# Kernel optimization log

Hardware: AMD Instinct MI355X
Metric: run time of the kernel (lower is better)

The kernel has to match this reference:

```python
import jax, jax.numpy as jnp
import numpy as np

KNOTS = 17

def _buffers():
    t = jnp.linspace(0.0, 3.0, KNOTS)                # (K,)
    dt = 3.0 / (KNOTS - 1)
    w = jnp.full((KNOTS,), 2.0 * dt)
    w = w.at[jnp.array([0, KNOTS - 1])].set(dt)      # trapezoid-like weights
    phi = jnp.exp(-t * t / 2.0)                      # standard normal CF
    return t, phi, w * phi


def setup_inputs() -> dict:
    key = jax.random.key(0)
    kz, ka = jax.random.split(key)
    n, d, num_proj = 8192, 768, 1024
    z = jax.random.normal(kz, (n, d), dtype=jnp.float32)
    a = jax.random.normal(ka, (d, num_proj), dtype=jnp.float32)
    return {"z": z, "a": a}


def reference(z, a):
    t, phi, weights = _buffers()
    # normalize projection directions (columns of a) to unit L2 norm
    a_n = a / jnp.linalg.norm(a, axis=0, keepdims=True)          # (d, P)
    proj = z @ a_n                                               # (n, P)
    x_t = proj[..., None] * t                                    # (n, P, K)
    cos_mean = jnp.cos(x_t).mean(axis=-3)                        # (P, K)
    sin_mean = jnp.sin(x_t).mean(axis=-3)                        # (P, K)
    err = (cos_mean - phi) ** 2 + sin_mean ** 2                  # (P, K)
    n = z.shape[-2]
    return (err @ weights * n).mean()                            # scalar
```

## Files before the change

kernel.cpp:

```cpp
#include <hip/hip_runtime.h>
#include <math.h>

typedef __attribute__((ext_vector_type(8))) short bf16x8;
typedef __attribute__((ext_vector_type(4))) float f32x4;

#define N_ROWS 8192
#define D_DIM  768
#define P_DIM  1024
#define KNOTS  17
#define NK     16
#define NCH    128
#define KSTEPS 12
#define ALD    72

__device__ inline unsigned short f2bf(float f) {
    union { float f; unsigned int u; } x; x.f = f;
    unsigned int r = x.u + 0x7FFFu + ((x.u >> 16) & 1u);
    return (unsigned short)(r >> 16);
}

__device__ inline bf16x8 pack8(float4 a, float4 b) {
    union { unsigned short s[8]; bf16x8 v; } r;
    r.s[0] = f2bf(a.x); r.s[1] = f2bf(a.y); r.s[2] = f2bf(a.z); r.s[3] = f2bf(a.w);
    r.s[4] = f2bf(b.x); r.s[5] = f2bf(b.y); r.s[6] = f2bf(b.z); r.s[7] = f2bf(b.w);
    return r.v;
}

__device__ inline void gload_lds16(const unsigned short* g, const unsigned short* l) {
    auto gp = reinterpret_cast<const __attribute__((address_space(1))) char*>(
        reinterpret_cast<uintptr_t>(g));
    auto lp = reinterpret_cast<__attribute__((address_space(3))) char*>(
        (uintptr_t)(unsigned int)reinterpret_cast<uintptr_t>(l));
    __builtin_amdgcn_global_load_lds(gp, lp, 16, 0, 0);
}

__global__ __launch_bounds__(256) void colsq_kernel(const float* __restrict__ a,
                                                    float* __restrict__ cpart) {
    int p  = blockIdx.x * 256 + threadIdx.x;
    int d0 = blockIdx.y * 64;
    float s = 0.f;
    for (int d = 0; d < 64; ++d) {
        float v = a[(size_t)(d0 + d) * P_DIM + p];
        s = fmaf(v, v, s);
    }
    cpart[(size_t)blockIdx.y * P_DIM + p] = s;
}

__global__ __launch_bounds__(256) void atconv_kernel(const float* __restrict__ a,
                                                     const float* __restrict__ cpart,
                                                     unsigned short* __restrict__ Bt) {
    __shared__ float tile[64][65];
    __shared__ float linv[64];
    const int d0 = blockIdx.x * 64, p0 = blockIdx.y * 64;
    const int tid = threadIdx.x;
    if (tid < 64) {
        float s = 0.f;
        #pragma unroll
        for (int j = 0; j < D_DIM / 64; ++j)
            s += cpart[(size_t)j * P_DIM + p0 + tid];
        linv[tid] = rsqrtf(s);
    }
    #pragma unroll
    for (int pass = 0; pass < 16; ++pass) {
        int idx = pass * 256 + tid;
        int dr = idx >> 6, pc = idx & 63;
        tile[dr][pc] = a[(size_t)(d0 + dr) * P_DIM + p0 + pc];
    }
    __syncthreads();
    #pragma unroll
    for (int pass = 0; pass < 16; ++pass) {
        int idx = pass * 256 + tid;
        int pr = idx >> 6, dc = idx & 63;
        Bt[(size_t)(p0 + pr) * D_DIM + d0 + dc] = f2bf(tile[dc][pr] * linv[pr]);
    }
}

__global__ __launch_bounds__(512, 4) void gemmcf_kernel(const float* __restrict__ Z,
                                                        const unsigned short* __restrict__ B,
                                                        float* __restrict__ part) {
    __shared__ unsigned short AsB[2][128 * ALD];
    __shared__ unsigned short BsB[2][128 * 64];
    const int tid  = threadIdx.x;
    const int lane = tid & 63;
    const int wave = tid >> 6;
    const int wr = wave >> 2, wc = wave & 3;

    const int bid = blockIdx.x + blockIdx.y * 8;
    const int swz = (bid & 7) * 64 + (bid >> 3);
    const int bx = swz & 7, by = swz >> 3;
    const int row0 = by * 128;
    const int col0 = bx * 128;

    const int aR = wave * 16 + (lane >> 2);
    const int ac = lane & 3;
    const float* Zg = Z + (size_t)(row0 + aR) * D_DIM + ac * 8;

    const int srow = wave * 16 + (lane >> 3);
    const int sc   = (lane & 7) ^ ((lane >> 3) & 7);
    const unsigned short* Bg = B + (size_t)(col0 + srow) * D_DIM + sc * 8;
    const int ldsw = wave * 16 * 64;

    float4 ar0, ar1, ar2, ar3;

#define ALOAD(kt) do { const float* zp_ = Zg + (kt) * 64;                    \
        ar0 = *reinterpret_cast<const float4*>(zp_);                         \
        ar1 = *reinterpret_cast<const float4*>(zp_ + 4);                     \
        ar2 = *reinterpret_cast<const float4*>(zp_ + 32);                    \
        ar3 = *reinterpret_cast<const float4*>(zp_ + 36); } while (0)
#define AWRITE(db) do {                                                      \
        *reinterpret_cast<bf16x8*>(&AsB[db][aR * ALD + ac * 8])       = pack8(ar0, ar1); \
        *reinterpret_cast<bf16x8*>(&AsB[db][aR * ALD + (ac + 4) * 8]) = pack8(ar2, ar3); } while (0)
#define BSTAGE(kt, db) do { const int k0_ = (kt) * 64;                       \
        gload_lds16(Bg + k0_,             &BsB[db][ldsw]);                   \
        gload_lds16(Bg + k0_ + 8 * D_DIM, &BsB[db][ldsw + 8 * 64]); } while (0)
#define DRAIN_BARRIER() do {                                                 \
        asm volatile("s_waitcnt vmcnt(0) lgkmcnt(0)" ::: "memory");          \
        __builtin_amdgcn_sched_barrier(0);                                   \
        __builtin_amdgcn_s_barrier(); } while (0)

    f32x4 acc[4][2] = {};

    ALOAD(0);
    AWRITE(0);
    BSTAGE(0, 0);
    ALOAD(1);
    DRAIN_BARRIER();

    #pragma unroll
    for (int t = 0; t < KSTEPS; ++t) {
        const int cur = t & 1;
        if (t + 1 < KSTEPS) {
            AWRITE(cur ^ 1);
            BSTAGE(t + 1, cur ^ 1);
            if (t + 2 < KSTEPS) ALOAD(t + 2);
        }
        #pragma unroll
        for (int kk = 0; kk < 2; ++kk) {
            bf16x8 af[4], bfr[2];
            const int kg = kk * 4 + (lane >> 4);
            const int kbp = (kg ^ (lane & 7)) * 8;
            #pragma unroll
            for (int mi = 0; mi < 4; ++mi)
                af[mi] = *reinterpret_cast<const bf16x8*>(
                    &AsB[cur][(wr * 64 + mi * 16 + (lane & 15)) * ALD + kg * 8]);
            #pragma unroll
            for (int ni = 0; ni < 2; ++ni)
                bfr[ni] = *reinterpret_cast<const bf16x8*>(
                    &BsB[cur][(wc * 32 + ni * 16 + (lane & 15)) * 64 + kbp]);
            #pragma unroll
            for (int mi = 0; mi < 4; ++mi)
                #pragma unroll
                for (int ni = 0; ni < 2; ++ni)
                    acc[mi][ni] = __builtin_amdgcn_mfma_f32_16x16x32_bf16(
                        af[mi], bfr[ni], acc[mi][ni], 0, 0, 0);
        }
        if (t + 1 < KSTEPS) DRAIN_BARRIER();
    }
#undef ALOAD
#undef AWRITE
#undef BSTAGE
#undef DRAIN_BARRIER

    const float dt = 0.1875f;
    #pragma unroll
    for (int ni = 0; ni < 2; ++ni) {
        float cs[NK], ss[NK];
        #pragma unroll
        for (int k = 0; k < NK; ++k) { cs[k] = 0.f; ss[k] = 0.f; }
        #pragma unroll
        for (int mi = 0; mi < 4; ++mi)
            #pragma unroll
            for (int j = 0; j < 4; ++j) {
                float th = acc[mi][ni][j] * dt;
                float s1 = __sinf(th);
                float c1 = __cosf(th);
                float c2 = 2.f * c1;
                float ckm2 = 1.f, skm2 = 0.f;
                float ckm1 = c1,  skm1 = s1;
                cs[0] += c1; ss[0] += s1;
                #pragma unroll
                for (int k = 2; k <= NK; ++k) {
                    float ck = fmaf(c2, ckm1, -ckm2);
                    float sk = fmaf(c2, skm1, -skm2);
                    cs[k - 1] += ck; ss[k - 1] += sk;
                    ckm2 = ckm1; skm2 = skm1;
                    ckm1 = ck;   skm1 = sk;
                }
            }
        #pragma unroll
        for (int k = 0; k < NK; ++k) {
            cs[k] += __shfl_xor(cs[k], 16);
            cs[k] += __shfl_xor(cs[k], 32);
            ss[k] += __shfl_xor(ss[k], 16);
            ss[k] += __shfl_xor(ss[k], 32);
        }
        if (lane < 16) {
            int col = col0 + wc * 32 + ni * 16 + lane;
            size_t base = ((size_t)(by * 2 + wr) * 2 * NK) * P_DIM + col;
            #pragma unroll
            for (int k = 0; k < NK; ++k) {
                part[base + (size_t)k * P_DIM]        = cs[k];
                part[base + (size_t)(NK + k) * P_DIM] = ss[k];
            }
        }
    }
}

__global__ __launch_bounds__(256) void red1_kernel(const float* __restrict__ part,
                                                   float* __restrict__ sums) {
    int g = blockIdx.x * 256 + threadIdx.x;
    float s = 0.f;
    for (int c = 0; c < NCH; ++c)
        s += part[(size_t)c * 2 * NK * P_DIM + g];
    sums[g] = s;
}

__global__ __launch_bounds__(1024) void red2_kernel(const float* __restrict__ sums,
                                                    float* __restrict__ out) {
    const int p = threadIdx.x;
    const float dt = 0.1875f;
    const float inv_n = 1.0f / (float)N_ROWS;
    float contrib = 0.f;
    #pragma unroll
    for (int k = 1; k <= NK; ++k) {
        float cm   = sums[(k - 1) * P_DIM + p] * inv_n;
        float sm   = sums[(NK + k - 1) * P_DIM + p] * inv_n;
        float tk   = dt * (float)k;
        float phik = expf(-0.5f * tk * tk);
        float wk   = (k == KNOTS - 1) ? dt : 2.f * dt;
        float d    = cm - phik;
        contrib += wk * phik * (d * d + sm * sm);
    }
    __shared__ float red[1024];
    red[p] = contrib;
    __syncthreads();
    for (int sft = 512; sft > 0; sft >>= 1) {
        if (p < sft) red[p] += red[p + sft];
        __syncthreads();
    }
    if (p == 0) out[0] = red[0] * (float)N_ROWS / (float)P_DIM;
}

extern "C" void kernel_launch(void* const* d_in, const int* in_sizes, int n_in,
                              void* d_out, int out_size, void* d_ws, size_t ws_size,
                              hipStream_t stream) {
    const float* z = (const float*)d_in[0];
    const float* a = (const float*)d_in[1];
    float* out = (float*)d_out;

    char* ws = (char*)d_ws;
    float*          cpart = (float*)ws;
    unsigned short* Bt    = (unsigned short*)(ws + 65536);
    float*          part  = (float*)(ws + 65536 + 1572864);
    float*          sums  = (float*)(ws + 65536 + 1572864 + 16777216);

    colsq_kernel<<<dim3(P_DIM / 256, D_DIM / 64), 256, 0, stream>>>(a, cpart);
    atconv_kernel<<<dim3(D_DIM / 64, P_DIM / 64), 256, 0, stream>>>(a, cpart, Bt);
    gemmcf_kernel<<<dim3(P_DIM / 128, N_ROWS / 128), 512, 0, stream>>>(z, Bt, part);
    red1_kernel<<<dim3(2 * NK * P_DIM / 256), 256, 0, stream>>>(part, sums);
    red2_kernel<<<1, 1024, 0, stream>>>(sums, out);
}
```

Measured before the change: 119.5 us.

## Load B fragments directly from global into registers, dropping LDS staging

Removes the LDS double buffer for the B operand. Each wave now loads its bf16 B fragments straight from global memory into registers every k-step. The barrier waits only on LDS counters, and the next A prefetch moves after the MFMAs. The fp32 to bf16 packing also switches to the HIP intrinsic. This cuts LDS traffic and the vmcnt drain at each barrier. In exchange, B global-load latency is exposed inside the loop with no prefetch, and waves sharing columns load the same data redundantly.

```diff
diff --git a/kernel.cpp b/kernel.cpp
--- a/kernel.cpp
+++ b/kernel.cpp
@@ -1,4 +1,5 @@
 #include <hip/hip_runtime.h>
+#include <hip/hip_bf16.h>
 #include <math.h>
 
 typedef __attribute__((ext_vector_type(8))) short bf16x8;
@@ -19,19 +20,16 @@
     return (unsigned short)(r >> 16);
 }
 
+__device__ inline unsigned short bfbits(float f) {
+    union { __hip_bfloat16 h; unsigned short u; } c;
+    c.h = __float2bfloat16(f);
+    return c.u;
+}
 __device__ inline bf16x8 pack8(float4 a, float4 b) {
     union { unsigned short s[8]; bf16x8 v; } r;
-    r.s[0] = f2bf(a.x); r.s[1] = f2bf(a.y); r.s[2] = f2bf(a.z); r.s[3] = f2bf(a.w);
-    r.s[4] = f2bf(b.x); r.s[5] = f2bf(b.y); r.s[6] = f2bf(b.z); r.s[7] = f2bf(b.w);
+    r.s[0] = bfbits(a.x); r.s[1] = bfbits(a.y); r.s[2] = bfbits(a.z); r.s[3] = bfbits(a.w);
+    r.s[4] = bfbits(b.x); r.s[5] = bfbits(b.y); r.s[6] = bfbits(b.z); r.s[7] = bfbits(b.w);
     return r.v;
-}
-
-__device__ inline void gload_lds16(const unsigned short* g, const unsigned short* l) {
-    auto gp = reinterpret_cast<const __attribute__((address_space(1))) char*>(
-        reinterpret_cast<uintptr_t>(g));
-    auto lp = reinterpret_cast<__attribute__((address_space(3))) char*>(
-        (uintptr_t)(unsigned int)reinterpret_cast<uintptr_t>(l));
-    __builtin_amdgcn_global_load_lds(gp, lp, 16, 0, 0);
 }
 
 __global__ __launch_bounds__(256) void colsq_kernel(const float* __restrict__ a,
@@ -79,7 +77,6 @@
                                                         const unsigned short* __restrict__ B,
                                                         float* __restrict__ part) {
     __shared__ unsigned short AsB[2][128 * ALD];
-    __shared__ unsigned short BsB[2][128 * 64];
     const int tid  = threadIdx.x;
     const int lane = tid & 63;
     const int wave = tid >> 6;
@@ -95,10 +92,9 @@
     const int ac = lane & 3;
     const float* Zg = Z + (size_t)(row0 + aR) * D_DIM + ac * 8;
 
-    const int srow = wave * 16 + (lane >> 3);
-    const int sc   = (lane & 7) ^ ((lane >> 3) & 7);
-    const unsigned short* Bg = B + (size_t)(col0 + srow) * D_DIM + sc * 8;
-    const int ldsw = wave * 16 * 64;
+    const unsigned short* Bg0 =
+        B + (size_t)(col0 + wc * 32 + (lane & 15)) * D_DIM + (lane >> 4) * 8;
+    const unsigned short* Bg1 = Bg0 + (size_t)16 * D_DIM;
 
     float4 ar0, ar1, ar2, ar3;
 
@@ -110,11 +106,8 @@
 #define AWRITE(db) do {                                                      \
         *reinterpret_cast<bf16x8*>(&AsB[db][aR * ALD + ac * 8])       = pack8(ar0, ar1); \
         *reinterpret_cast<bf16x8*>(&AsB[db][aR * ALD + (ac + 4) * 8]) = pack8(ar2, ar3); } while (0)
-#define BSTAGE(kt, db) do { const int k0_ = (kt) * 64;                       \
-        gload_lds16(Bg + k0_,             &BsB[db][ldsw]);                   \
-        gload_lds16(Bg + k0_ + 8 * D_DIM, &BsB[db][ldsw + 8 * 64]); } while (0)
-#define DRAIN_BARRIER() do {                                                 \
-        asm volatile("s_waitcnt vmcnt(0) lgkmcnt(0)" ::: "memory");          \
+#define LGKM_BARRIER() do {                                                  \
+        asm volatile("s_waitcnt lgkmcnt(0)" ::: "memory");                   \
         __builtin_amdgcn_sched_barrier(0);                                   \
         __builtin_amdgcn_s_barrier(); } while (0)
 
@@ -122,44 +115,41 @@
 
     ALOAD(0);
     AWRITE(0);
-    BSTAGE(0, 0);
     ALOAD(1);
-    DRAIN_BARRIER();
+    LGKM_BARRIER();
 
     #pragma unroll
     for (int t = 0; t < KSTEPS; ++t) {
         const int cur = t & 1;
-        if (t + 1 < KSTEPS) {
-            AWRITE(cur ^ 1);
-            BSTAGE(t + 1, cur ^ 1);
-            if (t + 2 < KSTEPS) ALOAD(t + 2);
-        }
+        if (t + 1 < KSTEPS) AWRITE(cur ^ 1);
+        const bf16x8 b00 = *reinterpret_cast<const bf16x8*>(Bg0 + t * 64);
+        const bf16x8 b01 = *reinterpret_cast<const bf16x8*>(Bg1 + t * 64);
+        const bf16x8 b10 = *reinterpret_cast<const bf16x8*>(Bg0 + t * 64 + 32);
+        const bf16x8 b11 = *reinterpret_cast<const bf16x8*>(Bg1 + t * 64 + 32);
         #pragma unroll
         for (int kk = 0; kk < 2; ++kk) {
-            bf16x8 af[4], bfr[2];
+            bf16x8 af[4];
             const int kg = kk * 4 + (lane >> 4);
-            const int kbp = (kg ^ (lane & 7)) * 8;
             #pragma unroll
             for (int mi = 0; mi < 4; ++mi)
                 af[mi] = *reinterpret_cast<const bf16x8*>(
                     &AsB[cur][(wr * 64 + mi * 16 + (lane & 15)) * ALD + kg * 8]);
-            #pragma unroll
-            for (int ni = 0; ni < 2; ++ni)
-                bfr[ni] = *reinterpret_cast<const bf16x8*>(
-                    &BsB[cur][(wc * 32 + ni * 16 + (lane & 15)) * 64 + kbp]);
-            #pragma unroll
-            for (int mi = 0; mi < 4; ++mi)
-                #pragma unroll
-                for (int ni = 0; ni < 2; ++ni)
-                    acc[mi][ni] = __builtin_amdgcn_mfma_f32_16x16x32_bf16(
-                        af[mi], bfr[ni], acc[mi][ni], 0, 0, 0);
+            const bf16x8 bn0 = kk ? b10 : b00;
+            const bf16x8 bn1 = kk ? b11 : b01;
+            #pragma unroll
+            for (int mi = 0; mi < 4; ++mi) {
+                acc[mi][0] = __builtin_amdgcn_mfma_f32_16x16x32_bf16(
+                    af[mi], bn0, acc[mi][0], 0, 0, 0);
+                acc[mi][1] = __builtin_amdgcn_mfma_f32_16x16x32_bf16(
+                    af[mi], bn1, acc[mi][1], 0, 0, 0);
+            }
         }
-        if (t + 1 < KSTEPS) DRAIN_BARRIER();
+        if (t + 2 < KSTEPS) ALOAD(t + 2);
+        if (t + 1 < KSTEPS) LGKM_BARRIER();
     }
 #undef ALOAD
 #undef AWRITE
-#undef BSTAGE
-#undef DRAIN_BARRIER
+#undef LGKM_BARRIER
 
     const float dt = 0.1875f;
     #pragma unroll
```

Measured after the change: 132.0 us. +10.5%, slower.
